# Optimization experiments

Measured on AMD Instinct MI355X. Metric: run time of the kernel, lower is better.

## Reference

```python
import jax, jax.numpy as jnp
import numpy as np

B, S, D, H = 1, 4096, 1024, 16
HD = D // H  # head_dim = 64


def setup_inputs() -> dict:
    key = jax.random.key(0)
    ks = jax.random.split(key, 5)
    scale = 1.0 / np.sqrt(D)
    return {
        "x_self": jax.random.normal(ks[0], (B, S, D), dtype=jnp.float32),
        "W_q": jax.random.normal(ks[1], (D, D), dtype=jnp.float32) * scale,
        "W_k": jax.random.normal(ks[2], (D, D), dtype=jnp.float32) * scale,
        "W_v": jax.random.normal(ks[3], (D, D), dtype=jnp.float32) * scale,
        "W_o": jax.random.normal(ks[4], (D, D), dtype=jnp.float32) * scale,
    }


def reference(x_self, W_q, W_k, W_v, W_o):
    b, s, d = x_self.shape
    # nn.Linear(bias=False): y = x @ W.T
    q = x_self @ W_q.T
    k = x_self @ W_k.T
    v = x_self @ W_v.T
    # [b, h, s, hd]
    q = q.reshape(b, s, H, HD).transpose(0, 2, 1, 3)
    k = k.reshape(b, s, H, HD).transpose(0, 2, 1, 3)
    v = v.reshape(b, s, H, HD).transpose(0, 2, 1, 3)
    scores = jnp.einsum("bhqd,bhkd->bhqk", q, k) / jnp.sqrt(jnp.float32(HD))
    # causal mask: -inf strictly above diagonal
    causal = jnp.triu(jnp.full((s, s), -jnp.inf, dtype=scores.dtype), k=1)
    scores = scores + causal[None, None, :, :]
    attn = jax.nn.softmax(scores.astype(jnp.float32), axis=-1).astype(q.dtype)
    ctx = jnp.einsum("bhqk,bhkd->bhqd", attn, v)  # [b, h, s, hd]
    out = ctx.transpose(0, 2, 1, 3).reshape(b, s, d)
    return out @ W_o.T
```

## Files before the change

kernel.cpp:

```cpp
#include <hip/hip_runtime.h>

typedef unsigned short u16;
typedef unsigned int u32;
typedef __attribute__((ext_vector_type(8))) short s16x8;
typedef __attribute__((ext_vector_type(4))) short s16x4;
typedef __attribute__((ext_vector_type(4))) float f32x4;

#define S_LEN 4096
#define D_DIM 1024
#define NH    16
#define HDIM  64
#define KVB   128

#define AS1 __attribute__((address_space(1)))
#define AS3 __attribute__((address_space(3)))

__device__ __forceinline__ u16 f2bf(float f) {
  unsigned u = __float_as_uint(f);
  u += 0x7FFF + ((u >> 16) & 1);
  return (u16)(u >> 16);
}

__device__ __forceinline__ u32 cvtpk2(float a, float b) {
  float r;
  asm("v_cvt_pk_bf16_f32 %0, %1, %2" : "=v"(r) : "v"(a), "v"(b));
  return __float_as_uint(r);
}

__device__ __forceinline__ u16 f2bf_pk(float f) {
  return (u16)(cvtpk2(f, f) & 0xffffu);
}

__device__ __forceinline__ float exp2fast(float x) {
  float r;
  asm("v_exp_f32 %0, %1" : "=v"(r) : "v"(x));
  return r;
}

__device__ __forceinline__ void load_lds16(const void* g, void* l) {
  __builtin_amdgcn_global_load_lds((AS1 void*)g, (AS3 void*)l, 16, 0, 0);
}

__device__ __forceinline__ unsigned lds_addr32(const void* p) {
  return (unsigned)(unsigned long long)(AS3 const char*)p;
}

__device__ __forceinline__ s16x4 ds_read_tr16(unsigned addr) {
  s16x4 r;
  asm volatile("ds_read_b64_tr_b16 %0, %1" : "=v"(r) : "v"(addr));
  return r;
}

__global__ __launch_bounds__(256) void cvt_bf16(const float* __restrict__ in,
                                                u16* __restrict__ out, int n) {
  int i = (blockIdx.x * 256 + threadIdx.x) * 4;
  if (i + 3 < n) {
    float4 v = *(const float4*)(in + i);
    ushort4 o;
    o.x = f2bf(v.x); o.y = f2bf(v.y); o.z = f2bf(v.z); o.w = f2bf(v.w);
    *(ushort4*)(out + i) = o;
  }
}

__global__ __launch_bounds__(256) void cvt_w4(const float* __restrict__ w0,
                                              const float* __restrict__ w1,
                                              const float* __restrict__ w2,
                                              const float* __restrict__ w3,
                                              u16* o0, u16* o1, u16* o2, u16* o3) {
  const float* in; u16* out;
  switch (blockIdx.y) {
    case 0: in = w0; out = o0; break;
    case 1: in = w1; out = o1; break;
    case 2: in = w2; out = o2; break;
    default: in = w3; out = o3; break;
  }
  int i = (blockIdx.x * 256 + threadIdx.x) * 4;
  float4 v = *(const float4*)(in + i);
  ushort4 o;
  o.x = f2bf(v.x); o.y = f2bf(v.y); o.z = f2bf(v.z); o.w = f2bf(v.w);
  *(ushort4*)(out + i) = o;
}

struct GemmSmem { u16 As[2][128 * 32]; u16 Bs[2][128 * 32]; };

template <bool BF16_OUT>
__device__ __forceinline__ void gemm_tile(GemmSmem& sm, const u16* __restrict__ A,
                                          const u16* __restrict__ B,
                                          void* __restrict__ C, int m0, int n0,
                                          int N, int K, float cscale) {
  const int t = threadIdx.x;
  const int l = t & 63, g = l >> 4, r = l & 15;
  const int w = t >> 6, wr = w >> 1, wc = w & 1;
  f32x4 acc[4][4] = {};
  const int swz = (g ^ ((r >> 1) & 3)) << 3;

  auto stage = [&](int buf, int k0) {
#pragma unroll
    for (int i = 0; i < 2; ++i) {
      const int gi = i * 256 + t;
      const int row = gi >> 2, cg = gi & 3;
      const int sc = cg ^ ((row >> 1) & 3);
      load_lds16(A + (size_t)(m0 + row) * K + k0 + sc * 8,
                 (char*)sm.As[buf] + (i * 256 + (t & 192)) * 16);
      load_lds16(B + (size_t)(n0 + row) * K + k0 + sc * 8,
                 (char*)sm.Bs[buf] + (i * 256 + (t & 192)) * 16);
    }
  };

  stage(0, 0);
  __syncthreads();
  int cur = 0;
  for (int k0 = 0; k0 < K; k0 += 32) {
    if (k0 + 32 < K) stage(cur ^ 1, k0 + 32);
    s16x8 a[4], b[4];
#pragma unroll
    for (int m = 0; m < 4; ++m)
      a[m] = *(const s16x8*)&sm.As[cur][(wr * 64 + m * 16 + r) * 32 + swz];
#pragma unroll
    for (int n = 0; n < 4; ++n)
      b[n] = *(const s16x8*)&sm.Bs[cur][(wc * 64 + n * 16 + r) * 32 + swz];
#pragma unroll
    for (int m = 0; m < 4; ++m)
#pragma unroll
      for (int n = 0; n < 4; ++n)
        acc[m][n] = __builtin_amdgcn_mfma_f32_16x16x32_bf16(a[m], b[n], acc[m][n], 0, 0, 0);
    __syncthreads();
    cur ^= 1;
  }
#pragma unroll
  for (int m = 0; m < 4; ++m)
#pragma unroll
    for (int n = 0; n < 4; ++n)
#pragma unroll
      for (int v = 0; v < 4; ++v) {
        int row = m0 + wr * 64 + m * 16 + g * 4 + v;
        int col = n0 + wc * 64 + n * 16 + r;
        float val = acc[m][n][v] * cscale;
        if (BF16_OUT)
          ((u16*)C)[(size_t)row * N + col] = f2bf_pk(val);
        else
          ((float*)C)[(size_t)row * N + col] = val;
      }
}

#define QSCALE 0.1803368801111204f

__global__ __launch_bounds__(256) void gemm_qkv(const u16* __restrict__ A,
                                                const u16* __restrict__ Bq,
                                                const u16* __restrict__ Bk,
                                                const u16* __restrict__ Bv,
                                                u16* Cq, u16* Ck, u16* Cv_) {
  __shared__ GemmSmem sm;
  const int which = blockIdx.x >> 3;
  const u16* B = which == 0 ? Bq : (which == 1 ? Bk : Bv);
  u16* C = which == 0 ? Cq : (which == 1 ? Ck : Cv_);
  const float cs = which == 0 ? QSCALE : 1.0f;
  gemm_tile<true>(sm, A, B, C, blockIdx.y * 128, (blockIdx.x & 7) * 128, D_DIM, D_DIM, cs);
}

__global__ __launch_bounds__(256) void gemm_out(const u16* __restrict__ A,
                                                const u16* __restrict__ B,
                                                float* __restrict__ C) {
  __shared__ GemmSmem sm;
  gemm_tile<false>(sm, A, B, C, blockIdx.y * 128, blockIdx.x * 128, D_DIM, D_DIM, 1.0f);
}

__global__ __launch_bounds__(256) void flash_attn(const u16* __restrict__ Q,
                                                  const u16* __restrict__ Kg,
                                                  const u16* __restrict__ V,
                                                  u16* __restrict__ CTX) {
  const int h = blockIdx.y;
  const int hoff = h * HDIM;
  const int t = threadIdx.x, w = t >> 6, l = t & 63, g = l >> 4, r = l & 15;

  __shared__ u16 Kt[2][KVB * 64];
  __shared__ u16 Vt[2][32 * 256];

  auto stage = [&](int buf, int kv0) {
#pragma unroll
    for (int i = 0; i < 4; ++i) {
      const int gi = i * 256 + t;
      const int krow = gi >> 3, c0 = gi & 7;
      load_lds16(Kg + (size_t)(kv0 + krow) * D_DIM + hoff + ((c0 ^ (krow & 7)) << 3),
                 (char*)Kt[buf] + (i * 256 + (t & 192)) * 16);
      const int sv = gi >> 5, vo = gi & 31;
      load_lds16(V + (size_t)(kv0 + (sv >> 2) * 16 + (vo >> 1)) * D_DIM + hoff +
                     (sv & 3) * 16 + (vo & 1) * 8,
                 (char*)Vt[buf] + (i * 256 + (t & 192)) * 16);
    }
  };

#pragma unroll 1
  for (int run = 0; run < 2; ++run) {
    const int qt = run == 0 ? (63 - (int)blockIdx.x) : (int)blockIdx.x;
    const int q0 = qt * 64 + w * 16;

    const u16* qrow = Q + (size_t)(q0 + r) * D_DIM + hoff;
    const s16x8 aq0 = *(const s16x8*)(qrow + g * 8);
    const s16x8 aq1 = *(const s16x8*)(qrow + 32 + g * 8);

    f32x4 o[4] = {};
    float mrun = -1e30f, lsum = 0.f;

    const int ntiles = (qt >> 1) + 1;
    stage(0, 0);
    __syncthreads();
    int cur = 0;

    for (int tile = 0; tile < ntiles; ++tile) {
      if (tile + 1 < ntiles) stage(cur ^ 1, (tile + 1) * KVB);
      const u16* Kb = Kt[cur];
      const bool lastT = (tile == ntiles - 1);

      f32x4 s[8];
      __builtin_amdgcn_s_setprio(1);
#pragma unroll
      for (int nb = 0; nb < 8; ++nb) {
        const int kr = nb * 16 + r;
        const int sw = kr & 7;
        s16x8 bk0 = *(const s16x8*)&Kb[kr * 64 + ((g ^ sw) << 3)];
        s16x8 bk1 = *(const s16x8*)&Kb[kr * 64 + (((4 + g) ^ sw) << 3)];
        f32x4 z = {0.f, 0.f, 0.f, 0.f};
        z = __builtin_amdgcn_mfma_f32_16x16x32_bf16(bk0, aq0, z, 0, 0, 0);
        z = __builtin_amdgcn_mfma_f32_16x16x32_bf16(bk1, aq1, z, 0, 0, 0);
        s[nb] = z;
      }
      __builtin_amdgcn_s_setprio(0);

      if (lastT) {
        const int qrel = q0 + r - tile * KVB;
#pragma unroll
        for (int nb = 0; nb < 8; ++nb)
#pragma unroll
          for (int j = 0; j < 4; ++j)
            if (16 * nb + 4 * g + j > qrel) s[nb][j] = -1e30f;
      }

      float tm = -1e30f;
#pragma unroll
      for (int nb = 0; nb < 8; ++nb) {
        float a0 = fmaxf(s[nb][0], s[nb][1]), a1 = fmaxf(s[nb][2], s[nb][3]);
        tm = fmaxf(tm, fmaxf(a0, a1));
      }
      tm = fmaxf(tm, __shfl_xor(tm, 16, 64));
      tm = fmaxf(tm, __shfl_xor(tm, 32, 64));
      const float mnew = fmaxf(mrun, tm);
      const float fs = exp2fast(mrun - mnew);
      mrun = mnew;
      float ps = 0.f;
#pragma unroll
      for (int nb = 0; nb < 8; ++nb)
#pragma unroll
        for (int j = 0; j < 4; ++j) {
          const float pv = exp2fast(s[nb][j] - mnew);
          s[nb][j] = pv;
          ps += pv;
        }
      ps += __shfl_xor(ps, 16, 64);
      ps += __shfl_xor(ps, 32, 64);
      lsum = lsum * fs + ps;
#pragma unroll
      for (int hb = 0; hb < 4; ++hb) {
        o[hb][0] *= fs; o[hb][1] *= fs; o[hb][2] *= fs; o[hb][3] *= fs;
      }

      s16x8 pa[4];
#pragma unroll
      for (int ks = 0; ks < 4; ++ks) {
        union { u32 u[4]; s16x8 v; } pk_;
        pk_.u[0] = cvtpk2(s[2 * ks][0],     s[2 * ks][1]);
        pk_.u[1] = cvtpk2(s[2 * ks][2],     s[2 * ks][3]);
        pk_.u[2] = cvtpk2(s[2 * ks + 1][0], s[2 * ks + 1][1]);
        pk_.u[3] = cvtpk2(s[2 * ks + 1][2], s[2 * ks + 1][3]);
        pa[ks] = pk_.v;
      }

      const unsigned vbase = lds_addr32(Vt[cur]) + (unsigned)(l * 8);
      s16x4 tv[4][4][2];
      auto issue_grp = [&](int ks) {
#pragma unroll
        for (int hb = 0; hb < 4; ++hb) {
          tv[ks][hb][0] = ds_read_tr16(vbase + (unsigned)(((2 * ks) * 4 + hb) * 512));
          tv[ks][hb][1] = ds_read_tr16(vbase + (unsigned)(((2 * ks + 1) * 4 + hb) * 512));
        }
      };
      issue_grp(0);
      issue_grp(1);
#pragma unroll
      for (int ks = 0; ks < 4; ++ks) {
        if (ks < 3) asm volatile("s_waitcnt lgkmcnt(8)" ::: "memory");
        else        asm volatile("s_waitcnt lgkmcnt(0)" ::: "memory");
        __builtin_amdgcn_sched_barrier(0);
        __builtin_amdgcn_s_setprio(1);
#pragma unroll
        for (int hb = 0; hb < 4; ++hb) {
          s16x8 vf = {tv[ks][hb][0][0], tv[ks][hb][0][1], tv[ks][hb][0][2], tv[ks][hb][0][3],
                      tv[ks][hb][1][0], tv[ks][hb][1][1], tv[ks][hb][1][2], tv[ks][hb][1][3]};
          o[hb] = __builtin_amdgcn_mfma_f32_16x16x32_bf16(vf, pa[ks], o[hb], 0, 0, 0);
        }
        __builtin_amdgcn_s_setprio(0);
        if (ks < 2) issue_grp(ks + 2);
      }
      __syncthreads();
      cur ^= 1;
    }

    const float inv = 1.0f / lsum;
    u16* crow = CTX + (size_t)(q0 + r) * D_DIM + hoff + 4 * g;
#pragma unroll
    for (int hb = 0; hb < 4; ++hb) {
      uint2 pk_;
      pk_.x = cvtpk2(o[hb][0] * inv, o[hb][1] * inv);
      pk_.y = cvtpk2(o[hb][2] * inv, o[hb][3] * inv);
      *(uint2*)(crow + hb * 16) = pk_;
    }
  }
}

extern "C" void kernel_launch(void* const* d_in, const int* in_sizes, int n_in,
                              void* d_out, int out_size, void* d_ws, size_t ws_size,
                              hipStream_t stream) {
  const float* x  = (const float*)d_in[0];
  const float* Wq = (const float*)d_in[1];
  const float* Wk = (const float*)d_in[2];
  const float* Wv = (const float*)d_in[3];
  const float* Wo = (const float*)d_in[4];

  u16* xb  = (u16*)d_ws;
  u16* Wqb = xb + (size_t)S_LEN * D_DIM;
  u16* Wkb = Wqb + (size_t)D_DIM * D_DIM;
  u16* Wvb = Wkb + (size_t)D_DIM * D_DIM;
  u16* Wob = Wvb + (size_t)D_DIM * D_DIM;
  u16* Qb  = Wob + (size_t)D_DIM * D_DIM;
  u16* Kb  = Qb + (size_t)S_LEN * D_DIM;
  u16* Vb  = Kb + (size_t)S_LEN * D_DIM;
  u16* Cb  = Vb + (size_t)S_LEN * D_DIM;

  cvt_bf16<<<S_LEN * D_DIM / 1024, 256, 0, stream>>>(x, xb, S_LEN * D_DIM);
  cvt_w4<<<dim3(D_DIM * D_DIM / 1024, 4), 256, 0, stream>>>(Wq, Wk, Wv, Wo,
                                                            Wqb, Wkb, Wvb, Wob);

  gemm_qkv<<<dim3(24, 32), 256, 0, stream>>>(xb, Wqb, Wkb, Wvb, Qb, Kb, Vb);
  flash_attn<<<dim3(32, NH), 256, 0, stream>>>(Qb, Kb, Vb, Cb);
  gemm_out<<<dim3(8, 32), 256, 0, stream>>>(Cb, Wob, (float*)d_out);
}
```

Baseline: 212.7 us.

## Widen flash-attention query blocks, fuse conversion kernels, and XCD-swizzle GEMM tiles

The flash-attention kernel now runs 512 threads per block over 128-row query tiles, so each staged K/V tile is shared by eight waves instead of four. The causal pairing of query tiles is kept. The two fp32-to-bf16 conversion kernels are merged into one launch, and both GEMMs remap block indices so neighbouring tiles land on the same XCD for better L2 reuse. The aim is to cut K/V staging traffic per unit of work, launch overhead and cross-die cache misses. The cost is larger blocks, which may lower occupancy or raise register pressure in attention.

After: 203.3 us. 4.4% less time.

```diff
diff --git a/kernel.cpp b/kernel.cpp
--- a/kernel.cpp
+++ b/kernel.cpp
@@ -11,6 +11,7 @@
 #define NH    16
 #define HDIM  64
 #define KVB   128
+#define QB    128
 
 #define AS1 __attribute__((address_space(1)))
 #define AS3 __attribute__((address_space(3)))
@@ -51,27 +52,21 @@
   return r;
 }
 
-__global__ __launch_bounds__(256) void cvt_bf16(const float* __restrict__ in,
-                                                u16* __restrict__ out, int n) {
-  int i = (blockIdx.x * 256 + threadIdx.x) * 4;
-  if (i + 3 < n) {
-    float4 v = *(const float4*)(in + i);
-    ushort4 o;
-    o.x = f2bf(v.x); o.y = f2bf(v.y); o.z = f2bf(v.z); o.w = f2bf(v.w);
-    *(ushort4*)(out + i) = o;
-  }
-}
-
-__global__ __launch_bounds__(256) void cvt_w4(const float* __restrict__ w0,
-                                              const float* __restrict__ w1,
-                                              const float* __restrict__ w2,
-                                              const float* __restrict__ w3,
-                                              u16* o0, u16* o1, u16* o2, u16* o3) {
+__global__ __launch_bounds__(256) void cvt_all(const float* __restrict__ x,
+                                               const float* __restrict__ w0,
+                                               const float* __restrict__ w1,
+                                               const float* __restrict__ w2,
+                                               const float* __restrict__ w3,
+                                               u16* xb, u16* o0, u16* o1,
+                                               u16* o2, u16* o3) {
   const float* in; u16* out;
-  switch (blockIdx.y) {
-    case 0: in = w0; out = o0; break;
-    case 1: in = w1; out = o1; break;
-    case 2: in = w2; out = o2; break;
+  const int slab = blockIdx.y;
+  switch (slab) {
+    case 0: case 1: case 2: case 3:
+      in = x + (size_t)slab * D_DIM * 1024; out = xb + (size_t)slab * D_DIM * 1024; break;
+    case 4: in = w0; out = o0; break;
+    case 5: in = w1; out = o1; break;
+    case 6: in = w2; out = o2; break;
     default: in = w3; out = o3; break;
   }
   int i = (blockIdx.x * 256 + threadIdx.x) * 4;
@@ -151,21 +146,26 @@
                                                 const u16* __restrict__ Bv,
                                                 u16* Cq, u16* Ck, u16* Cv_) {
   __shared__ GemmSmem sm;
-  const int which = blockIdx.x >> 3;
+  const int f = blockIdx.y * 24 + blockIdx.x;
+  const int tid = (f & 7) * 96 + (f >> 3);
+  const int nby = tid / 24, nbx = tid % 24;
+  const int which = nbx >> 3;
   const u16* B = which == 0 ? Bq : (which == 1 ? Bk : Bv);
   u16* C = which == 0 ? Cq : (which == 1 ? Ck : Cv_);
   const float cs = which == 0 ? QSCALE : 1.0f;
-  gemm_tile<true>(sm, A, B, C, blockIdx.y * 128, (blockIdx.x & 7) * 128, D_DIM, D_DIM, cs);
+  gemm_tile<true>(sm, A, B, C, nby * 128, (nbx & 7) * 128, D_DIM, D_DIM, cs);
 }
 
 __global__ __launch_bounds__(256) void gemm_out(const u16* __restrict__ A,
                                                 const u16* __restrict__ B,
                                                 float* __restrict__ C) {
   __shared__ GemmSmem sm;
-  gemm_tile<false>(sm, A, B, C, blockIdx.y * 128, blockIdx.x * 128, D_DIM, D_DIM, 1.0f);
-}
-
-__global__ __launch_bounds__(256) void flash_attn(const u16* __restrict__ Q,
+  const int f = blockIdx.y * 8 + blockIdx.x;
+  const int tid = (f & 7) * 32 + (f >> 3);
+  gemm_tile<false>(sm, A, B, C, (tid >> 3) * 128, (tid & 7) * 128, D_DIM, D_DIM, 1.0f);
+}
+
+__global__ __launch_bounds__(512) void flash_attn(const u16* __restrict__ Q,
                                                   const u16* __restrict__ Kg,
                                                   const u16* __restrict__ V,
                                                   u16* __restrict__ CTX) {
@@ -178,22 +178,22 @@
 
   auto stage = [&](int buf, int kv0) {
 #pragma unroll
-    for (int i = 0; i < 4; ++i) {
-      const int gi = i * 256 + t;
+    for (int i = 0; i < 2; ++i) {
+      const int gi = i * 512 + t;
       const int krow = gi >> 3, c0 = gi & 7;
       load_lds16(Kg + (size_t)(kv0 + krow) * D_DIM + hoff + ((c0 ^ (krow & 7)) << 3),
-                 (char*)Kt[buf] + (i * 256 + (t & 192)) * 16);
+                 (char*)Kt[buf] + (i * 512 + (t & 448)) * 16);
       const int sv = gi >> 5, vo = gi & 31;
       load_lds16(V + (size_t)(kv0 + (sv >> 2) * 16 + (vo >> 1)) * D_DIM + hoff +
                      (sv & 3) * 16 + (vo & 1) * 8,
-                 (char*)Vt[buf] + (i * 256 + (t & 192)) * 16);
+                 (char*)Vt[buf] + (i * 512 + (t & 448)) * 16);
     }
   };
 
 #pragma unroll 1
   for (int run = 0; run < 2; ++run) {
-    const int qt = run == 0 ? (63 - (int)blockIdx.x) : (int)blockIdx.x;
-    const int q0 = qt * 64 + w * 16;
+    const int qt = run == 0 ? (31 - (int)blockIdx.x) : (int)blockIdx.x;
+    const int q0 = qt * QB + w * 16;
 
     const u16* qrow = Q + (size_t)(q0 + r) * D_DIM + hoff;
     const s16x8 aq0 = *(const s16x8*)(qrow + g * 8);
@@ -202,7 +202,7 @@
     f32x4 o[4] = {};
     float mrun = -1e30f, lsum = 0.f;
 
-    const int ntiles = (qt >> 1) + 1;
+    const int ntiles = qt + 1;
     stage(0, 0);
     __syncthreads();
     int cur = 0;
@@ -336,11 +336,9 @@
   u16* Vb  = Kb + (size_t)S_LEN * D_DIM;
   u16* Cb  = Vb + (size_t)S_LEN * D_DIM;
 
-  cvt_bf16<<<S_LEN * D_DIM / 1024, 256, 0, stream>>>(x, xb, S_LEN * D_DIM);
-  cvt_w4<<<dim3(D_DIM * D_DIM / 1024, 4), 256, 0, stream>>>(Wq, Wk, Wv, Wo,
-                                                            Wqb, Wkb, Wvb, Wob);
-
+  cvt_all<<<dim3(1024, 8), 256, 0, stream>>>(x, Wq, Wk, Wv, Wo,
+                                             xb, Wqb, Wkb, Wvb, Wob);
   gemm_qkv<<<dim3(24, 32), 256, 0, stream>>>(xb, Wqb, Wkb, Wvb, Qb, Kb, Vb);
-  flash_attn<<<dim3(32, NH), 256, 0, stream>>>(Qb, Kb, Vb, Cb);
+  flash_attn<<<dim3(S_LEN / QB / 2, NH), 512, 0, stream>>>(Qb, Kb, Vb, Cb);
   gemm_out<<<dim3(8, 32), 256, 0, stream>>>(Cb, Wob, (float*)d_out);
 }
```
